# Optimization experiments

Measured on AMD Instinct MI355X. Metric: run time of the kernel, lower is better.

Reference implementation:

```python
import jax, jax.numpy as jnp
import numpy as np

_COOR = [[1,4],[1,5],[1,6],[2,4],[2,6],[3,1],[3,2],[3,3],[3,4],[3,5],[3,6],[3,7],[3,8],[3,9],[4,1],[4,2],[4,3],[4,4],[4,5],[4,6],[4,7],[4,8],[4,9],[5,1],[5,2],[5,3],[5,4],[5,5],[5,6],[5,7],[5,8],[5,9],[6,1],[6,2],[6,3],[6,4],[6,5],[6,6],[6,7],[6,8],[6,9],[7,1],[7,2],[7,3],[7,4],[7,5],[7,6],[7,7],[7,8],[7,9],[8,2],[8,3],[8,4],[8,5],[8,6],[8,7],[8,8],[9,3],[9,4],[9,5],[9,6],[9,7]]
_DIRS = [[1,2,3,4,5,6,7,8,9,10,11,12,13,14,15,16,17,18,19,20,21,22,23,24,25,26,27,28,29,30,31,32,33,34,35,36,37,38,39,40,41,42,43,44,45,46,47,48,49,50,58,52,53,54,55,56,62,60,61,51,57,59],[59,57,51,61,60,62,56,55,54,53,52,58,50,41,32,23,14,49,40,31,22,13,48,39,30,21,12,47,38,29,20,11,46,37,28,19,10,45,36,27,18,9,44,35,26,17,8,43,34,25,16,7,42,33,24,15,6,5,4,3,2,1],[59,57,51,61,60,62,56,55,54,53,52,58,50,49,48,47,46,45,44,43,42,41,40,39,38,37,36,35,34,33,32,31,30,29,28,27,26,25,24,23,22,21,20,19,18,17,16,15,14,13,12,11,10,9,8,7,6,5,4,3,2,1],[1,2,3,4,5,6,15,24,33,42,7,16,25,34,43,8,17,26,35,44,9,18,27,36,45,10,19,28,37,46,11,20,29,38,47,12,21,30,39,48,13,22,31,40,49,14,23,32,41,50,58,52,53,54,55,56,62,60,61,51,57,59]]


def _build_graph():
    D, E = len(_DIRS), len(_COOR)
    Ns = np.zeros((D, E, E), np.float32)
    for di, direction in enumerate(_DIRS):
        for pi in range(E):
            i, j = _COOR[direction[pi] - 1]
            nbrs = {0: [[i, j - 1], [i - 1, j - 1], [i - 1, j]],
                    1: [[i, j + 1], [i - 1, j], [i - 1, j + 1]],
                    2: [[i, j - 1], [i + 1, j - 1], [i + 1, j]],
                    3: [[i, j - 1], [i - 1, j - 1], [i - 1, j]]}[di]
            for nb in nbrs:
                if nb in _COOR:
                    n_idx = _COOR.index(nb) + 1
                    if n_idx in direction[:pi]:
                        Ns[di, pi, direction.index(n_idx)] = 1.0
    perm = np.asarray(_DIRS, np.int32) - 1  # [D,E] electrode index visited at each step
    return jnp.asarray(Ns), jnp.asarray(perm)


def _srnn(x_t, Ns, perm, U_w, U_b, W_w, W_b, sp_bs, P_w, P_b, ps_w, ps_b):
    # x_t: [B,E,C] -> m: [B,HID]
    B, E, _ = x_t.shape
    HID = U_b.shape[1]

    def one_dir(ns, pm, uw, ub, ww, wb, b, pw, pb):
        ux = jnp.einsum('bec,hc->beh', x_t[:, pm], uw) + ub  # [B,E,H] precomputed input term
        H0 = jnp.zeros((B, E, ub.shape[0]), x_t.dtype)

        def step(H, inp):
            ns_row, ux_pi, pi = inp
            # ns_row is nonzero only at already-visited step positions (< pi)
            h_agg = jnp.einsum('e,beh->bh', ns_row, H)
            h = jax.nn.relu(ux_pi + h_agg @ ww.T + wb + b)
            return jax.lax.dynamic_update_slice(H, h[:, None, :], (0, pi, 0)), None

        H, _ = jax.lax.scan(step, H0, (ns, jnp.swapaxes(ux, 0, 1), jnp.arange(E)))
        return jnp.einsum('beh,pe->bhp', H, pw) + pb  # [B,H,P]

    s = jax.vmap(one_dir)(Ns, perm, U_w, U_b, W_w, W_b, sp_bs, P_w, P_b)  # [D,B,H,P]
    s = jnp.moveaxis(s, 0, 2).reshape(B, HID, -1)  # [B,H,D*P]
    return (s @ ps_w.T + ps_b)[..., 0]  # [B,H]


def _trnn(ms, rs_w, rs_b, vs_w, vs_b, bs, pj_w, pj_b):
    # ms: [T,B,H]
    h0 = jnp.zeros(ms.shape[1:], ms.dtype)

    def step(h, m_t):
        h = jax.nn.relu(m_t @ rs_w.T + rs_b + h @ vs_w.T + vs_b + bs)
        return h, h

    _, hs = jax.lax.scan(step, h0, ms)  # [T,B,H]
    return jnp.einsum('tbh,pt->bph', hs, pj_w) + pj_b[None, :, None]  # [B,P,H]


def _forward(x, Ns, perm, U_w, U_b, W_w, W_b, sp_bs, P_w, P_b, ps_w, ps_b,
             f_rs_w, f_rs_b, f_vs_w, f_vs_b, f_bs, f_pj_w, f_pj_b,
             b_rs_w, b_rs_b, b_vs_w, b_vs_b, b_bs, b_pj_w, b_pj_b,
             fp1_w, fp1_b, fp2_w, fp2_b, bp1_w, bp1_b, bp2_w, bp2_b):
    xt = jnp.swapaxes(x, 0, 1)  # [T,B,E,C]
    ms = jax.vmap(lambda xi: _srnn(xi, Ns, perm, U_w, U_b, W_w, W_b, sp_bs,
                                   P_w, P_b, ps_w, ps_b))(xt)  # [T,B,H]
    q_f = _trnn(ms, f_rs_w, f_rs_b, f_vs_w, f_vs_b, f_bs, f_pj_w, f_pj_b)
    q_b = _trnn(ms[::-1], b_rs_w, b_rs_b, b_vs_w, b_vs_b, b_bs, b_pj_w, b_pj_b)
    zf = (q_f @ fp1_w.T + fp1_b)[..., 0]  # [B,Ptp]
    zb = (q_b @ bp1_w.T + bp1_b)[..., 0]
    return zf @ fp2_w.T + fp2_b + zb @ bp2_w.T + bp2_b  # [B,classes]


def setup_inputs() -> dict:
    B, T, E, C = 128, 16, 62, 5
    HID, SPP, TPP, NC, D = 128, 16, 8, 3, 4
    Ns, perm = _build_graph()
    key = jax.random.key(0)
    ks = jax.random.split(key, 34)
    rnd = lambda k, s: (jax.random.normal(k, s, jnp.float32) * 0.05)
    return {
        'x': jax.random.normal(ks[0], (B, T, E, C), jnp.float32),
        'Ns': Ns, 'perm': perm,
        'U_w': rnd(ks[1], (D, HID, C)), 'U_b': rnd(ks[2], (D, HID)),
        'W_w': rnd(ks[3], (D, HID, HID)), 'W_b': rnd(ks[4], (D, HID)),
        'sp_bs': rnd(ks[5], (D, HID)),
        'P_w': rnd(ks[6], (D, SPP, E)), 'P_b': rnd(ks[7], (D, SPP)),
        'ps_w': rnd(ks[8], (1, D * SPP)), 'ps_b': rnd(ks[9], (1,)),
        'f_rs_w': rnd(ks[10], (HID, HID)), 'f_rs_b': rnd(ks[11], (HID,)),
        'f_vs_w': rnd(ks[12], (HID, HID)), 'f_vs_b': rnd(ks[13], (HID,)),
        'f_bs': rnd(ks[14], (HID,)),
        'f_pj_w': rnd(ks[15], (TPP, T)), 'f_pj_b': rnd(ks[16], (TPP,)),
        'b_rs_w': rnd(ks[17], (HID, HID)), 'b_rs_b': rnd(ks[18], (HID,)),
        'b_vs_w': rnd(ks[19], (HID, HID)), 'b_vs_b': rnd(ks[20], (HID,)),
        'b_bs': rnd(ks[21], (HID,)),
        'b_pj_w': rnd(ks[22], (TPP, T)), 'b_pj_b': rnd(ks[23], (TPP,)),
        'fp1_w': rnd(ks[24], (1, HID)), 'fp1_b': rnd(ks[25], (1,)),
        'fp2_w': rnd(ks[26], (NC, TPP)), 'fp2_b': rnd(ks[27], (NC,)),
        'bp1_w': rnd(ks[28], (1, HID)), 'bp1_b': rnd(ks[29], (1,)),
        'bp2_w': rnd(ks[30], (NC, TPP)), 'bp2_b': rnd(ks[31], (NC,)),
    }


def reference(x, Ns, perm, U_w, U_b, W_w, W_b, sp_bs, P_w, P_b, ps_w, ps_b,
              f_rs_w, f_rs_b, f_vs_w, f_vs_b, f_bs, f_pj_w, f_pj_b,
              b_rs_w, b_rs_b, b_vs_w, b_vs_b, b_bs, b_pj_w, b_pj_b,
              fp1_w, fp1_b, fp2_w, fp2_b, bp1_w, bp1_b, bp2_w, bp2_b):
    return _forward(x, Ns, perm, U_w, U_b, W_w, W_b, sp_bs, P_w, P_b, ps_w, ps_b,
                    f_rs_w, f_rs_b, f_vs_w, f_vs_b, f_bs, f_pj_w, f_pj_b,
                    b_rs_w, b_rs_b, b_vs_w, b_vs_b, b_bs, b_pj_w, b_pj_b,
                    fp1_w, fp1_b, fp2_w, fp2_b, bp1_w, bp1_b, bp2_w, bp2_b)
```

## Files before the change

### kernel.cpp

```cpp
#include <hip/hip_runtime.h>

typedef unsigned short u16;
typedef unsigned int   u32;

using bf16x8 = __attribute__((ext_vector_type(8))) short;
using f32x4  = __attribute__((ext_vector_type(4))) float;
using u32x4  = __attribute__((ext_vector_type(4))) unsigned;

__device__ __forceinline__ u32 cvtpk(float lo, float hi) {
  u32 r;
  asm("v_cvt_pk_bf16_f32 %0, %1, %2" : "=v"(r) : "v"(lo), "v"(hi));
  return r;
}
__device__ __forceinline__ bf16x8 pack8(float f0,float f1,float f2,float f3,
                                        float f4,float f5,float f6,float f7) {
  u32x4 t; t[0]=cvtpk(f0,f1); t[1]=cvtpk(f2,f3); t[2]=cvtpk(f4,f5); t[3]=cvtpk(f6,f7);
  return __builtin_bit_cast(bf16x8, t);
}
__device__ __forceinline__ u16 f2bf(float f) {
  u32 u = __float_as_uint(f);
  u32 r = u + 0x7FFFu + ((u >> 16) & 1u);
  return (u16)(r >> 16);
}

struct Sched {
  unsigned v[4][64];
  unsigned char opi[4][64];
  int nslot;
};

constexpr int cCOOR[62][2] = {
  {1,4},{1,5},{1,6},{2,4},{2,6},
  {3,1},{3,2},{3,3},{3,4},{3,5},{3,6},{3,7},{3,8},{3,9},
  {4,1},{4,2},{4,3},{4,4},{4,5},{4,6},{4,7},{4,8},{4,9},
  {5,1},{5,2},{5,3},{5,4},{5,5},{5,6},{5,7},{5,8},{5,9},
  {6,1},{6,2},{6,3},{6,4},{6,5},{6,6},{6,7},{6,8},{6,9},
  {7,1},{7,2},{7,3},{7,4},{7,5},{7,6},{7,7},{7,8},{7,9},
  {8,2},{8,3},{8,4},{8,5},{8,6},{8,7},{8,8},
  {9,3},{9,4},{9,5},{9,6},{9,7}};

constexpr int cDIRS[4][62] = {
  {1,2,3,4,5,6,7,8,9,10,11,12,13,14,15,16,17,18,19,20,21,22,23,24,25,26,27,28,29,30,
   31,32,33,34,35,36,37,38,39,40,41,42,43,44,45,46,47,48,49,50,
   58,52,53,54,55,56,62,60,61,51,57,59},
  {59,57,51,61,60,62,56,55,54,53,52,58,50,41,32,23,14,49,40,31,22,13,48,39,30,21,12,
   47,38,29,20,11,46,37,28,19,10,45,36,27,18,9,44,35,26,17,8,43,34,25,16,7,42,33,24,
   15,6,5,4,3,2,1},
  {59,57,51,61,60,62,56,55,54,53,52,58,50,49,48,47,46,45,44,43,42,41,40,39,38,37,36,
   35,34,33,32,31,30,29,28,27,26,25,24,23,22,21,20,19,18,17,16,15,14,13,12,11,10,9,
   8,7,6,5,4,3,2,1},
  {1,2,3,4,5,6,15,24,33,42,7,16,25,34,43,8,17,26,35,44,9,18,27,36,45,10,19,28,37,46,
   11,20,29,38,47,12,21,30,39,48,13,22,31,40,49,14,23,32,41,50,
   58,52,53,54,55,56,62,60,61,51,57,59}};

constexpr int cOFFS[4][3][2] = {
  {{0,-1},{-1,-1},{-1,0}},
  {{0, 1},{-1, 0},{-1,1}},
  {{0,-1},{ 1,-1},{ 1,0}},
  {{0,-1},{-1,-1},{-1,0}}};

constexpr Sched make_sched() {
  Sched S{};
  int nslot_all = 0;
  for (int d = 0; d < 4; ++d) {
    int pos_of[63] = {};
    for (int p = 0; p < 62; ++p) pos_of[cDIRS[d][p]] = p;
    int nb[62][3] = {}; int nc[62] = {}; int rdcnt[62] = {};
    for (int p = 0; p < 62; ++p) {
      const int e = cDIRS[d][p];
      const int ci = cCOOR[e-1][0], cj = cCOOR[e-1][1];
      for (int o = 0; o < 3; ++o) {
        const int ni = ci + cOFFS[d][o][0], nj = cj + cOFFS[d][o][1];
        int q = 0;
        for (int k2 = 0; k2 < 62; ++k2)
          if (cCOOR[k2][0]==ni && cCOOR[k2][1]==nj) { q = k2+1; break; }
        if (q) { const int qp = pos_of[q];
          if (qp < p) { nb[p][nc[p]] = qp; nc[p] = nc[p]+1; rdcnt[qp] = rdcnt[qp]+1; } }
      }
    }
    int lvl[62] = {};
    for (int p = 0; p < 62; ++p) {
      int m = 0;
      for (int o = 0; o < nc[p]; ++o) if (lvl[nb[p][o]] > m) m = lvl[nb[p][o]];
      lvl[p] = m + 1;
    }
    int ord[62] = {}; int k = 0;
    for (int L = 1; L <= 62; ++L)
      for (int p = 0; p < 62; ++p) if (lvl[p] == L) { ord[k] = p; k = k+1; }
    int slotof[62] = {};
    int rl[20]; int lr[20];
    for (int s = 0; s < 20; ++s) { rl[s] = 0; lr[s] = -1; }
    int nslot = 0, cur_sub = 0;
    int barafter[62] = {};
    int prev_lvl = lvl[ord[0]];
    for (int kk = 0; kk < 62; ++kk) {
      const int p = ord[kk];
      if (lvl[p] != prev_lvl) { barafter[kk-1] = 1; cur_sub = cur_sub+1; prev_lvl = lvl[p]; }
      for (int o = 0; o < nc[p]; ++o) {
        const int s = slotof[nb[p][o]];
        rl[s] = rl[s]-1;
        if (cur_sub > lr[s]) lr[s] = cur_sub;
      }
      int myslot = 31;
      if (rdcnt[p] > 0) {
        int found = -1;
        for (int s = 0; s < nslot; ++s)
          if (rl[s] == 0 && lr[s] < cur_sub) { found = s; break; }
        if (found < 0 && nslot < 19) { found = nslot; nslot = nslot+1; }
        if (found < 0) {
          barafter[kk-1] = 1; cur_sub = cur_sub+1;
          for (int o = 0; o < nc[p]; ++o) {
            const int s = slotof[nb[p][o]];
            if (cur_sub > lr[s]) lr[s] = cur_sub;
          }
          for (int s = 0; s < nslot; ++s)
            if (rl[s] == 0 && lr[s] < cur_sub) { found = s; break; }
        }
        if (found < 0 && nslot < 20) { found = nslot; nslot = nslot+1; }
        if (found < 0) found = 0;
        myslot = found;
        rl[myslot] = rdcnt[p];
        lr[myslot] = -1;
        slotof[p] = myslot;
      }
      S.opi[d][kk] = (unsigned char)p;
      S.v[d][kk] = (unsigned)(cDIRS[d][p]-1)
                 | ((unsigned)myslot << 6)
                 | ((unsigned)nc[p] << 11)
                 | ((unsigned)(nc[p]>0 ? slotof[nb[p][0]] : 0) << 13)
                 | ((unsigned)(nc[p]>1 ? slotof[nb[p][1]] : 0) << 18)
                 | ((unsigned)(nc[p]>2 ? slotof[nb[p][2]] : 0) << 23);
    }
    for (int kk = 0; kk < 62; ++kk) if (barafter[kk]) S.v[d][kk] |= (1u << 28);
    if (nslot > nslot_all) nslot_all = nslot;
  }
  S.nslot = nslot_all;
  return S;
}

constexpr Sched g_sched = make_sched();
static_assert(g_sched.nslot >= 8 && g_sched.nslot <= 20, "slot pressure out of range");
__constant__ Sched c_sched = make_sched();

constexpr int POOL_B     = g_sched.nslot * 4096;
constexpr int WP_OFF     = POOL_B;
constexpr int SRNN_SMEM  = POOL_B + 256;

__global__ __launch_bounds__(256, 2) void srnn_kernel(
    const float* __restrict__ x,    const float* __restrict__ Uw,
    const float* __restrict__ Ub,   const float* __restrict__ Ww,
    const float* __restrict__ Wb,   const float* __restrict__ spbs,
    const float* __restrict__ Pw,   const float* __restrict__ psw,
    float* __restrict__ part)
{
  extern __shared__ __align__(16) char smem[];
  const int tid  = threadIdx.x;
  const int lane = tid & 63, wid = tid >> 6;
  const int l15  = lane & 15, lhi = lane >> 4;
  const int bx = blockIdx.x;
  const int bb = bx & 15, d = (bx >> 4) & 3, tp = bx >> 6;
  const int b0 = bb * 8, t0 = tp * 2;

  float* s_wp = (float*)(smem + WP_OFF);

  if (tid < 62) {
    const int opi = c_sched.opi[d][tid];
    float acc = 0.f;
    for (int q = 0; q < 16; ++q) acc += Pw[(d * 16 + q) * 62 + opi] * psw[d * 16 + q];
    s_wp[tid] = acc;
  }

  bf16x8 wf[2][4];
  float bias[2];
#pragma unroll
  for (int nt = 0; nt < 2; ++nt) {
    const int n = wid * 32 + nt * 16 + l15;
    const float* wr = Ww + (size_t)(d * 128 + n) * 128;
#pragma unroll
    for (int kc = 0; kc < 4; ++kc) {
      float4 lo = *(const float4*)(wr + kc * 32 + lhi * 4);
      float4 hi = *(const float4*)(wr + kc * 32 + lhi * 4 + 16);
      wf[nt][kc] = pack8(lo.x, hi.x, lo.y, hi.y, lo.z, hi.z, lo.w, hi.w);
    }
    bias[nt] = Ub[d * 128 + n] + Wb[d * 128 + n] + spbs[d * 128 + n];
  }

  float u0a=0,u1a=0,u2a=0,u3a=0,u4a=0, u0b=0,u1b=0,u2b=0,u3b=0,u4b=0;
  if (lhi == 0) {
    const float* ua = Uw + (d * 128 + wid * 32 + l15) * 5;
    const float* ub = Uw + (d * 128 + wid * 32 + 16 + l15) * 5;
    u0a=ua[0]; u1a=ua[1]; u2a=ua[2]; u3a=ua[3]; u4a=ua[4];
    u0b=ub[0]; u1b=ub[1]; u2b=ub[2]; u3b=ub[3]; u4b=ub[4];
  }
  const bf16x8 uwf0 = pack8(u0a,u1a,u2a,u3a,u4a,0.f,0.f,0.f);
  const bf16x8 uwf1 = pack8(u0b,u1b,u2b,u3b,u4b,0.f,0.f,0.f);

  __syncthreads();

  const float* xlane = x + (size_t)((b0 + (l15 & 7)) * 16 + (t0 + (l15 >> 3))) * 310;
  const int swz_r = ((l15 & 7) << 4);
  const int wcol  = wid * 64 + l15 * 4;
  const unsigned* scv = c_sched.v[d];

  f32x4 macc0 = {0.f,0.f,0.f,0.f}, macc1 = {0.f,0.f,0.f,0.f};

  auto do_step = [&](unsigned sv, int kidx, float c0, float c1, float c2, float c3, float c4) {
    f32x4 a0 = {bias[0], bias[0], bias[0], bias[0]};
    f32x4 a1 = {bias[1], bias[1], bias[1], bias[1]};
    const int nbc = (int)((sv >> 11) & 3u);
    auto slot_mac = [&](int sl) {
      const char* sb = smem + sl * 4096 + l15 * 256;
#pragma unroll
      for (int kc = 0; kc < 4; ++kc) {
        bf16x8 a = *(const bf16x8*)(sb + ((kc * 64 + lhi * 16) ^ swz_r));
        a0 = __builtin_amdgcn_mfma_f32_16x16x32_bf16(a, wf[0][kc], a0, 0, 0, 0);
        a1 = __builtin_amdgcn_mfma_f32_16x16x32_bf16(a, wf[1][kc], a1, 0, 0, 0);
      }
    };
    if (nbc > 0) slot_mac((int)((sv >> 13) & 31u));
    if (nbc > 1) slot_mac((int)((sv >> 18) & 31u));
    if (nbc > 2) slot_mac((int)((sv >> 23) & 31u));
    bf16x8 xa = pack8(c0, c1, c2, c3, c4, 0.f, 0.f, 0.f);
    a0 = __builtin_amdgcn_mfma_f32_16x16x32_bf16(xa, uwf0, a0, 0, 0, 0);
    a1 = __builtin_amdgcn_mfma_f32_16x16x32_bf16(xa, uwf1, a1, 0, 0, 0);

    const int snew = (int)((sv >> 6) & 31u);
    const float wp = s_wp[kidx];
    float h0r[4], h1r[4];
#pragma unroll
    for (int r = 0; r < 4; ++r) { h0r[r] = fmaxf(a0[r], 0.f); h1r[r] = fmaxf(a1[r], 0.f); }
    if (snew != 31) {
      char* dst = smem + snew * 4096;
#pragma unroll
      for (int r = 0; r < 4; ++r) {
        const int row = lhi * 4 + r;
        *(u32*)(dst + row * 256 + (wcol ^ ((row & 7) << 4))) = cvtpk(h0r[r], h1r[r]);
      }
    }
#pragma unroll
    for (int r = 0; r < 4; ++r) { macc0[r] += h0r[r] * wp; macc1[r] += h1r[r] * wp; }
  };

  for (int pp = 0; pp < 31; ++pp) {
    const unsigned svA = scv[2 * pp];
    const unsigned svB = scv[2 * pp + 1];
    float a0=0,a1=0,a2=0,a3=0,a4=0, b0f=0,b1f=0,b2f=0,b3f=0,b4f=0;
    if (lhi == 0) {
      const float* pA = xlane + (svA & 63u) * 5;
      const float* pB = xlane + (svB & 63u) * 5;
      a0=pA[0]; a1=pA[1]; a2=pA[2]; a3=pA[3]; a4=pA[4];
      b0f=pB[0]; b1f=pB[1]; b2f=pB[2]; b3f=pB[3]; b4f=pB[4];
    }
    do_step(svA, 2 * pp, a0, a1, a2, a3, a4);
    if (svA & (1u << 28)) __syncthreads();
    do_step(svB, 2 * pp + 1, b0f, b1f, b2f, b3f, b4f);
    if (svB & (1u << 28)) __syncthreads();
  }

#pragma unroll
  for (int r = 0; r < 4; ++r) {
    const int row = lhi * 4 + r;
    const int t = t0 + (row >> 3);
    const int brow = b0 + (row & 7);
    const int n0 = wid * 32 + l15;
    float* pp2 = part + (((size_t)d * 16 + t) * 128 + brow) * 128;
    pp2[n0]      = macc0[r];
    pp2[n0 + 16] = macc1[r];
  }
}

constexpr int MS_OFF = 0;
constexpr int HB_OFF = 65536;
constexpr int SW_OFF = HB_OFF + 8704;
constexpr int S2_OFF = SW_OFF + 4096;
constexpr int TRNN_SMEM = S2_OFF + 1024;

__global__ __launch_bounds__(256) void trnn_kernel(
    const float* __restrict__ part, const float* __restrict__ Pb,
    const float* __restrict__ psw,  const float* __restrict__ psb,
    const float* __restrict__ frs, const float* __restrict__ frsb,
    const float* __restrict__ fvs, const float* __restrict__ fvsb,
    const float* __restrict__ fbs, const float* __restrict__ fpj, const float* __restrict__ fpjb,
    const float* __restrict__ brs, const float* __restrict__ brsb,
    const float* __restrict__ bvs, const float* __restrict__ bvsb,
    const float* __restrict__ bbs, const float* __restrict__ bpj, const float* __restrict__ bpjb,
    const float* __restrict__ fp1w, const float* __restrict__ fp1b,
    const float* __restrict__ fp2w, const float* __restrict__ fp2b,
    const float* __restrict__ bp1w, const float* __restrict__ bp1b,
    const float* __restrict__ bp2w, const float* __restrict__ bp2b,
    float* __restrict__ out)
{
  extern __shared__ __align__(16) char smem[];
  const int tid = threadIdx.x;
  const int lane = tid & 63, wid = tid >> 6;
  const int l15 = lane & 15, lhi = lane >> 4;
  const int dir = blockIdx.x & 1;
  const int b0 = (blockIdx.x >> 1) * 16;

  const float* rs  = dir ? brs  : frs;
  const float* rsb = dir ? brsb : frsb;
  const float* vs  = dir ? bvs  : fvs;
  const float* vsb = dir ? bvsb : fvsb;
  const float* bs  = dir ? bbs  : fbs;
  const float* w1  = dir ? bp1w : fp1w;

  {
    const int tq = tid >> 4, bq = tid & 15;
    float c0 = psb[0];
#pragma unroll
    for (int i = 0; i < 16; ++i) {
      float4 pb4 = *(const float4*)(Pb + i * 4);
      float4 pw4 = *(const float4*)(psw + i * 4);
      c0 += pb4.x*pw4.x + pb4.y*pw4.y + pb4.z*pw4.z + pb4.w*pw4.w;
    }
    const size_t base = ((size_t)tq * 128 + b0 + bq) * 128;
    const float* p0 = part + base;
    const float* p1 = part + base + 262144;
    const float* p2 = part + base + 2 * 262144;
    const float* p3 = part + base + 3 * 262144;
    char* mrow = smem + MS_OFF + (tq * 16 + bq) * 256;
    const int sz = (bq & 7) << 4;
    for (int h4 = 0; h4 < 32; ++h4) {
      float4 v0 = *(const float4*)(p0 + h4 * 4);
      float4 v1 = *(const float4*)(p1 + h4 * 4);
      float4 v2 = *(const float4*)(p2 + h4 * 4);
      float4 v3 = *(const float4*)(p3 + h4 * 4);
      float s0 = v0.x + v1.x + v2.x + v3.x + c0;
      float s1 = v0.y + v1.y + v2.y + v3.y + c0;
      float s2 = v0.z + v1.z + v2.z + v3.z + c0;
      float s3 = v0.w + v1.w + v2.w + v3.w + c0;
      *(u32*)(mrow + ((h4 * 8) ^ sz))     = cvtpk(s0, s1);
      *(u32*)(mrow + ((h4 * 8 + 4) ^ sz)) = cvtpk(s2, s3);
    }
  }

  bf16x8 rf[2][4], vf[2][4];
  float bias[2], w1a, w1b;
#pragma unroll
  for (int nt = 0; nt < 2; ++nt) {
    const int n = wid * 32 + nt * 16 + l15;
#pragma unroll
    for (int kc = 0; kc < 4; ++kc) {
      float4 ra = *(const float4*)(rs + (size_t)n * 128 + kc * 32 + lhi * 8);
      float4 rb = *(const float4*)(rs + (size_t)n * 128 + kc * 32 + lhi * 8 + 4);
      rf[nt][kc] = pack8(ra.x, ra.y, ra.z, ra.w, rb.x, rb.y, rb.z, rb.w);
      float4 lo = *(const float4*)(vs + (size_t)n * 128 + kc * 32 + lhi * 4);
      float4 hi = *(const float4*)(vs + (size_t)n * 128 + kc * 32 + lhi * 4 + 16);
      vf[nt][kc] = pack8(lo.x, hi.x, lo.y, hi.y, lo.z, hi.z, lo.w, hi.w);
    }
    bias[nt] = rsb[n] + vsb[n] + bs[n];
  }
  w1a = w1[wid * 32 + l15];
  w1b = w1[wid * 32 + 16 + l15];

  for (int i = tid; i < 2176; i += 256) *(u16*)(smem + HB_OFF + i * 2) = 0;
  __syncthreads();

  float* sredw = (float*)(smem + SW_OFF);
  float* sred2 = (float*)(smem + S2_OFF);

  int cur = 0;
  for (int tt2 = 0; tt2 < 16; ++tt2) {
    const int tt = dir ? (15 - tt2) : tt2;
    f32x4 am0 = {bias[0],bias[0],bias[0],bias[0]};
    f32x4 am1 = {bias[1],bias[1],bias[1],bias[1]};
    f32x4 ah0 = {0.f,0.f,0.f,0.f}, ah1 = {0.f,0.f,0.f,0.f};
    const char* msrow = smem + MS_OFF + (tt * 16 + l15) * 256;
    const int msz = (l15 & 7) << 4;
#pragma unroll
    for (int kc = 0; kc < 4; ++kc) {
      bf16x8 ma = *(const bf16x8*)(msrow + ((kc * 64 + lhi * 16) ^ msz));
      bf16x8 ha = *(const bf16x8*)(smem + HB_OFF + (cur * 16 + l15) * 272 + kc * 64 + lhi * 16);
      am0 = __builtin_amdgcn_mfma_f32_16x16x32_bf16(ma, rf[0][kc], am0, 0, 0, 0);
      ah0 = __builtin_amdgcn_mfma_f32_16x16x32_bf16(ha, vf[0][kc], ah0, 0, 0, 0);
      am1 = __builtin_amdgcn_mfma_f32_16x16x32_bf16(ma, rf[1][kc], am1, 0, 0, 0);
      ah1 = __builtin_amdgcn_mfma_f32_16x16x32_bf16(ha, vf[1][kc], ah1, 0, 0, 0);
    }
    float pr[4];
#pragma unroll
    for (int r = 0; r < 4; ++r) {
      const int row = lhi * 4 + r;
      float h0 = fmaxf(am0[r] + ah0[r], 0.f);
      float h1 = fmaxf(am1[r] + ah1[r], 0.f);
      *(u32*)(smem + HB_OFF + ((cur ^ 1) * 16 + row) * 272 + wid * 64 + l15 * 4) = cvtpk(h0, h1);
      pr[r] = h0 * w1a + h1 * w1b;
    }
#pragma unroll
    for (int r = 0; r < 4; ++r) {
      float p = pr[r];
      p += __shfl_xor(p, 1);
      p += __shfl_xor(p, 2);
      p += __shfl_xor(p, 4);
      p += __shfl_xor(p, 8);
      if (l15 == 0) sredw[(tt2 * 16 + lhi * 4 + r) * 4 + wid] = p;
    }
    __syncthreads();
    cur ^= 1;
  }

  {
    const int tq = tid >> 4, bq = tid & 15;
    const float* sw = sredw + (tq * 16 + bq) * 4;
    sred2[tq * 16 + bq] = sw[0] + sw[1] + sw[2] + sw[3];
  }
  __syncthreads();

  if (tid < 48) {
    const int b = tid / 3, c = tid % 3;
    const float* p1w = dir ? bp1w : fp1w;
    const float* p1b = dir ? bp1b : fp1b;
    const float* p2w = dir ? bp2w : fp2w;
    const float* p2b = dir ? bp2b : fp2b;
    const float* pj  = dir ? bpj  : fpj;
    const float* pjb = dir ? bpjb : fpjb;
    float S1 = 0.f;
    for (int h = 0; h < 128; ++h) S1 += p1w[h];
    float val = p2b[c];
    for (int p = 0; p < 8; ++p) val += (pjb[p] * S1 + p1b[0]) * p2w[c * 8 + p];
    for (int t2 = 0; t2 < 16; ++t2) {
      float g = 0.f;
      for (int p = 0; p < 8; ++p) g += p2w[c * 8 + p] * pj[p * 16 + t2];
      val += sred2[t2 * 16 + b] * g;
    }
    atomicAdd(out + (b0 + b) * 3 + c, val);
  }
}

extern "C" void kernel_launch(void* const* d_in, const int* in_sizes, int n_in,
                              void* d_out, int out_size, void* d_ws, size_t ws_size,
                              hipStream_t stream)
{
  (void)in_sizes; (void)n_in; (void)ws_size;
  const float* x    = (const float*)d_in[0];
  const float* Uw   = (const float*)d_in[3];
  const float* Ub   = (const float*)d_in[4];
  const float* Ww   = (const float*)d_in[5];
  const float* Wb   = (const float*)d_in[6];
  const float* spbs = (const float*)d_in[7];
  const float* Pw   = (const float*)d_in[8];
  const float* Pb   = (const float*)d_in[9];
  const float* psw  = (const float*)d_in[10];
  const float* psb  = (const float*)d_in[11];
  const float* frs  = (const float*)d_in[12];
  const float* frsb = (const float*)d_in[13];
  const float* fvs  = (const float*)d_in[14];
  const float* fvsb = (const float*)d_in[15];
  const float* fbs  = (const float*)d_in[16];
  const float* fpj  = (const float*)d_in[17];
  const float* fpjb = (const float*)d_in[18];
  const float* brs  = (const float*)d_in[19];
  const float* brsb = (const float*)d_in[20];
  const float* bvs  = (const float*)d_in[21];
  const float* bvsb = (const float*)d_in[22];
  const float* bbs  = (const float*)d_in[23];
  const float* bpj  = (const float*)d_in[24];
  const float* bpjb = (const float*)d_in[25];
  const float* fp1w = (const float*)d_in[26];
  const float* fp1b = (const float*)d_in[27];
  const float* fp2w = (const float*)d_in[28];
  const float* fp2b = (const float*)d_in[29];
  const float* bp1w = (const float*)d_in[30];
  const float* bp1b = (const float*)d_in[31];
  const float* bp2w = (const float*)d_in[32];
  const float* bp2b = (const float*)d_in[33];

  float* part = (float*)d_ws;

  hipFuncSetAttribute((const void*)srnn_kernel,
                      hipFuncAttributeMaxDynamicSharedMemorySize, SRNN_SMEM);
  hipFuncSetAttribute((const void*)trnn_kernel,
                      hipFuncAttributeMaxDynamicSharedMemorySize, TRNN_SMEM);

  hipMemsetAsync(d_out, 0, (size_t)out_size * sizeof(float), stream);

  srnn_kernel<<<dim3(512), dim3(256), SRNN_SMEM, stream>>>(
      x, Uw, Ub, Ww, Wb, spbs, Pw, psw, part);
  trnn_kernel<<<dim3(16), dim3(256), TRNN_SMEM, stream>>>(part, Pb, psw, psb,
      frs, frsb, fvs, fvsb, fbs, fpj, fpjb,
      brs, brsb, bvs, bvsb, bbs, bpj, bpjb,
      fp1w, fp1b, fp2w, fp2b, bp1w, bp1b, bp2w, bp2b,
      (float*)d_out);
}
```

Before: 89.67 us.

## Fully unroll SRNN schedule at compile time and split partial reduction into kernel

```diff
diff --git a/kernel.cpp b/kernel.cpp
--- a/kernel.cpp
+++ b/kernel.cpp
@@ -1,4 +1,5 @@
 #include <hip/hip_runtime.h>
+#include <utility>
 
 typedef unsigned short u16;
 typedef unsigned int   u32;
@@ -142,120 +143,177 @@
 static_assert(g_sched.nslot >= 8 && g_sched.nslot <= 20, "slot pressure out of range");
 __constant__ Sched c_sched = make_sched();
 
-constexpr int POOL_B     = g_sched.nslot * 4096;
-constexpr int WP_OFF     = POOL_B;
-constexpr int SRNN_SMEM  = POOL_B + 256;
-
-__global__ __launch_bounds__(256, 2) void srnn_kernel(
-    const float* __restrict__ x,    const float* __restrict__ Uw,
-    const float* __restrict__ Ub,   const float* __restrict__ Ww,
-    const float* __restrict__ Wb,   const float* __restrict__ spbs,
-    const float* __restrict__ Pw,   const float* __restrict__ psw,
-    float* __restrict__ part)
+constexpr int POOL_B    = g_sched.nslot * 4096;
+constexpr int SRNN_SMEM = POOL_B + 256;
+
+template <int D, int K>
+__device__ __forceinline__ void do_step(
+    char* smem, const float* s_wp,
+    const bf16x8 (&wf)[2][4], const bf16x8& uwf0, const bf16x8& uwf1,
+    float bias0, float bias1,
+    const u32 (&xr)[16][3], const int (&bad)[4],
+    const u32 (&rdv)[4], const u32 (&wav)[4],
+    f32x4& macc0, f32x4& macc1)
+{
+  constexpr unsigned sv = g_sched.v[D][K];
+  constexpr int snew = (int)((sv >> 6) & 31u);
+  constexpr int nbc  = (int)((sv >> 11) & 3u);
+  constexpr int sl0  = (int)((sv >> 13) & 31u);
+  constexpr int sl1  = (int)((sv >> 18) & 31u);
+  constexpr int sl2  = (int)((sv >> 23) & 31u);
+  constexpr int g    = K & 3;
+  constexpr int js   = K >> 2;
+
+  u32 r0 = (u32)__builtin_amdgcn_ds_bpermute(bad[g], (int)xr[js][0]);
+  u32 r1 = (u32)__builtin_amdgcn_ds_bpermute(bad[g], (int)xr[js][1]);
+  u32 r2 = (u32)__builtin_amdgcn_ds_bpermute(bad[g], (int)xr[js][2]);
+
+  f32x4 a0 = {bias0, bias0, bias0, bias0};
+  f32x4 a1 = {bias1, bias1, bias1, bias1};
+
+  if constexpr (nbc > 0) {
+#pragma unroll
+    for (int kc = 0; kc < 4; ++kc) {
+      bf16x8 a = *(const bf16x8*)(smem + sl0 * 4096 + rdv[kc]);
+      a0 = __builtin_amdgcn_mfma_f32_16x16x32_bf16(a, wf[0][kc], a0, 0, 0, 0);
+      a1 = __builtin_amdgcn_mfma_f32_16x16x32_bf16(a, wf[1][kc], a1, 0, 0, 0);
+    }
+  }
+  if constexpr (nbc > 1) {
+#pragma unroll
+    for (int kc = 0; kc < 4; ++kc) {
+      bf16x8 a = *(const bf16x8*)(smem + sl1 * 4096 + rdv[kc]);
+      a0 = __builtin_amdgcn_mfma_f32_16x16x32_bf16(a, wf[0][kc], a0, 0, 0, 0);
+      a1 = __builtin_amdgcn_mfma_f32_16x16x32_bf16(a, wf[1][kc], a1, 0, 0, 0);
+    }
+  }
+  if constexpr (nbc > 2) {
+#pragma unroll
+    for (int kc = 0; kc < 4; ++kc) {
+      bf16x8 a = *(const bf16x8*)(smem + sl2 * 4096 + rdv[kc]);
+      a0 = __builtin_amdgcn_mfma_f32_16x16x32_bf16(a, wf[0][kc], a0, 0, 0, 0);
+      a1 = __builtin_amdgcn_mfma_f32_16x16x32_bf16(a, wf[1][kc], a1, 0, 0, 0);
+    }
+  }
+  {
+    u32x4 xv; xv[0] = r0; xv[1] = r1; xv[2] = r2; xv[3] = 0;
+    bf16x8 xa = __builtin_bit_cast(bf16x8, xv);
+    a0 = __builtin_amdgcn_mfma_f32_16x16x32_bf16(xa, uwf0, a0, 0, 0, 0);
+    a1 = __builtin_amdgcn_mfma_f32_16x16x32_bf16(xa, uwf1, a1, 0, 0, 0);
+  }
+
+  const float wp = s_wp[K];
+  float h0[4], h1[4];
+#pragma unroll
+  for (int r = 0; r < 4; ++r) { h0[r] = fmaxf(a0[r], 0.f); h1[r] = fmaxf(a1[r], 0.f); }
+  if constexpr (snew != 31) {
+#pragma unroll
+    for (int r = 0; r < 4; ++r)
+      *(u32*)(smem + snew * 4096 + wav[r]) = cvtpk(h0[r], h1[r]);
+  }
+#pragma unroll
+  for (int r = 0; r < 4; ++r) { macc0[r] += h0[r] * wp; macc1[r] += h1[r] * wp; }
+
+  if constexpr ((sv >> 28) & 1u) __syncthreads();
+}
+
+template <int D, int... Ks>
+__device__ __forceinline__ void run_steps(
+    std::integer_sequence<int, Ks...>,
+    char* smem, const float* s_wp,
+    const bf16x8 (&wf)[2][4], const bf16x8& uwf0, const bf16x8& uwf1,
+    float bias0, float bias1,
+    const u32 (&xr)[16][3], const int (&bad)[4],
+    const u32 (&rdv)[4], const u32 (&wav)[4],
+    f32x4& macc0, f32x4& macc1)
+{
+  (do_step<D, Ks>(smem, s_wp, wf, uwf0, uwf1, bias0, bias1,
+                  xr, bad, rdv, wav, macc0, macc1), ...);
+}
+
+template <int D>
+__device__ __noinline__ void srnn_body(
+    const float* __restrict__ x,  const float* __restrict__ Uw,
+    const float* __restrict__ Ub, const float* __restrict__ Ww,
+    const float* __restrict__ Wb, const float* __restrict__ spbs,
+    const float* __restrict__ Pw, const float* __restrict__ psw,
+    float* __restrict__ part, int bx)
 {
   extern __shared__ __align__(16) char smem[];
   const int tid  = threadIdx.x;
   const int lane = tid & 63, wid = tid >> 6;
   const int l15  = lane & 15, lhi = lane >> 4;
-  const int bx = blockIdx.x;
-  const int bb = bx & 15, d = (bx >> 4) & 3, tp = bx >> 6;
+  const int bb = bx & 15, tp = bx >> 6;
   const int b0 = bb * 8, t0 = tp * 2;
 
-  float* s_wp = (float*)(smem + WP_OFF);
+  float* s_wp = (float*)(smem + POOL_B);
 
   if (tid < 62) {
-    const int opi = c_sched.opi[d][tid];
+    const int opi = c_sched.opi[D][tid];
     float acc = 0.f;
-    for (int q = 0; q < 16; ++q) acc += Pw[(d * 16 + q) * 62 + opi] * psw[d * 16 + q];
+    for (int q = 0; q < 16; ++q) acc += Pw[(D * 16 + q) * 62 + opi] * psw[D * 16 + q];
     s_wp[tid] = acc;
   }
 
   bf16x8 wf[2][4];
-  float bias[2];
+  float bias0, bias1;
 #pragma unroll
   for (int nt = 0; nt < 2; ++nt) {
     const int n = wid * 32 + nt * 16 + l15;
-    const float* wr = Ww + (size_t)(d * 128 + n) * 128;
+    const float* wr = Ww + (size_t)(D * 128 + n) * 128;
 #pragma unroll
     for (int kc = 0; kc < 4; ++kc) {
       float4 lo = *(const float4*)(wr + kc * 32 + lhi * 4);
       float4 hi = *(const float4*)(wr + kc * 32 + lhi * 4 + 16);
       wf[nt][kc] = pack8(lo.x, hi.x, lo.y, hi.y, lo.z, hi.z, lo.w, hi.w);
     }
-    bias[nt] = Ub[d * 128 + n] + Wb[d * 128 + n] + spbs[d * 128 + n];
+    float bnt = Ub[D * 128 + n] + Wb[D * 128 + n] + spbs[D * 128 + n];
+    if (nt == 0) bias0 = bnt; else bias1 = bnt;
   }
 
   float u0a=0,u1a=0,u2a=0,u3a=0,u4a=0, u0b=0,u1b=0,u2b=0,u3b=0,u4b=0;
   if (lhi == 0) {
-    const float* ua = Uw + (d * 128 + wid * 32 + l15) * 5;
-    const float* ub = Uw + (d * 128 + wid * 32 + 16 + l15) * 5;
+    const float* ua = Uw + (D * 128 + wid * 32 + l15) * 5;
+    const float* ub = Uw + (D * 128 + wid * 32 + 16 + l15) * 5;
     u0a=ua[0]; u1a=ua[1]; u2a=ua[2]; u3a=ua[3]; u4a=ua[4];
     u0b=ub[0]; u1b=ub[1]; u2b=ub[2]; u3b=ub[3]; u4b=ub[4];
   }
   const bf16x8 uwf0 = pack8(u0a,u1a,u2a,u3a,u4a,0.f,0.f,0.f);
   const bf16x8 uwf1 = pack8(u0b,u1b,u2b,u3b,u4b,0.f,0.f,0.f);
 
+  const float* xlane = x + (size_t)((b0 + (l15 & 7)) * 16 + (t0 + (l15 >> 3))) * 310;
+  u32 xr[16][3];
+#pragma unroll
+  for (int j = 0; j < 16; ++j) {
+    const int e = (int)(c_sched.v[D][j * 4 + lhi] & 63u);
+    const float* xp = xlane + e * 5;
+    float x0 = xp[0], x1 = xp[1], x2 = xp[2], x3 = xp[3], x4 = xp[4];
+    xr[j][0] = cvtpk(x0, x1);
+    xr[j][1] = cvtpk(x2, x3);
+    xr[j][2] = cvtpk(x4, 0.f);
+  }
+
+  const int swz_r = ((l15 & 7) << 4);
+  u32 rdv[4], wav[4];
+#pragma unroll
+  for (int kc = 0; kc < 4; ++kc)
+    rdv[kc] = (u32)(l15 * 256 + ((kc * 64 + lhi * 16) ^ swz_r));
+  const int wcol = wid * 64 + l15 * 4;
+#pragma unroll
+  for (int r = 0; r < 4; ++r) {
+    const int row = lhi * 4 + r;
+    wav[r] = (u32)(row * 256 + (wcol ^ ((row & 7) << 4)));
+  }
+  int bad[4];
+#pragma unroll
+  for (int i = 0; i < 4; ++i) bad[i] = (i * 16 + l15) * 4;
+
   __syncthreads();
 
-  const float* xlane = x + (size_t)((b0 + (l15 & 7)) * 16 + (t0 + (l15 >> 3))) * 310;
-  const int swz_r = ((l15 & 7) << 4);
-  const int wcol  = wid * 64 + l15 * 4;
-  const unsigned* scv = c_sched.v[d];
-
   f32x4 macc0 = {0.f,0.f,0.f,0.f}, macc1 = {0.f,0.f,0.f,0.f};
-
-  auto do_step = [&](unsigned sv, int kidx, float c0, float c1, float c2, float c3, float c4) {
-    f32x4 a0 = {bias[0], bias[0], bias[0], bias[0]};
-    f32x4 a1 = {bias[1], bias[1], bias[1], bias[1]};
-    const int nbc = (int)((sv >> 11) & 3u);
-    auto slot_mac = [&](int sl) {
-      const char* sb = smem + sl * 4096 + l15 * 256;
-#pragma unroll
-      for (int kc = 0; kc < 4; ++kc) {
-        bf16x8 a = *(const bf16x8*)(sb + ((kc * 64 + lhi * 16) ^ swz_r));
-        a0 = __builtin_amdgcn_mfma_f32_16x16x32_bf16(a, wf[0][kc], a0, 0, 0, 0);
-        a1 = __builtin_amdgcn_mfma_f32_16x16x32_bf16(a, wf[1][kc], a1, 0, 0, 0);
-      }
-    };
-    if (nbc > 0) slot_mac((int)((sv >> 13) & 31u));
-    if (nbc > 1) slot_mac((int)((sv >> 18) & 31u));
-    if (nbc > 2) slot_mac((int)((sv >> 23) & 31u));
-    bf16x8 xa = pack8(c0, c1, c2, c3, c4, 0.f, 0.f, 0.f);
-    a0 = __builtin_amdgcn_mfma_f32_16x16x32_bf16(xa, uwf0, a0, 0, 0, 0);
-    a1 = __builtin_amdgcn_mfma_f32_16x16x32_bf16(xa, uwf1, a1, 0, 0, 0);
-
-    const int snew = (int)((sv >> 6) & 31u);
-    const float wp = s_wp[kidx];
-    float h0r[4], h1r[4];
-#pragma unroll
-    for (int r = 0; r < 4; ++r) { h0r[r] = fmaxf(a0[r], 0.f); h1r[r] = fmaxf(a1[r], 0.f); }
-    if (snew != 31) {
-      char* dst = smem + snew * 4096;
-#pragma unroll
-      for (int r = 0; r < 4; ++r) {
-        const int row = lhi * 4 + r;
-        *(u32*)(dst + row * 256 + (wcol ^ ((row & 7) << 4))) = cvtpk(h0r[r], h1r[r]);
-      }
-    }
-#pragma unroll
-    for (int r = 0; r < 4; ++r) { macc0[r] += h0r[r] * wp; macc1[r] += h1r[r] * wp; }
-  };
-
-  for (int pp = 0; pp < 31; ++pp) {
-    const unsigned svA = scv[2 * pp];
-    const unsigned svB = scv[2 * pp + 1];
-    float a0=0,a1=0,a2=0,a3=0,a4=0, b0f=0,b1f=0,b2f=0,b3f=0,b4f=0;
-    if (lhi == 0) {
-      const float* pA = xlane + (svA & 63u) * 5;
-      const float* pB = xlane + (svB & 63u) * 5;
-      a0=pA[0]; a1=pA[1]; a2=pA[2]; a3=pA[3]; a4=pA[4];
-      b0f=pB[0]; b1f=pB[1]; b2f=pB[2]; b3f=pB[3]; b4f=pB[4];
-    }
-    do_step(svA, 2 * pp, a0, a1, a2, a3, a4);
-    if (svA & (1u << 28)) __syncthreads();
-    do_step(svB, 2 * pp + 1, b0f, b1f, b2f, b3f, b4f);
-    if (svB & (1u << 28)) __syncthreads();
-  }
+  run_steps<D>(std::make_integer_sequence<int, 62>{},
+               smem, s_wp, wf, uwf0, uwf1, bias0, bias1,
+               xr, bad, rdv, wav, macc0, macc1);
 
 #pragma unroll
   for (int r = 0; r < 4; ++r) {
@@ -263,10 +321,43 @@
     const int t = t0 + (row >> 3);
     const int brow = b0 + (row & 7);
     const int n0 = wid * 32 + l15;
-    float* pp2 = part + (((size_t)d * 16 + t) * 128 + brow) * 128;
-    pp2[n0]      = macc0[r];
-    pp2[n0 + 16] = macc1[r];
-  }
+    float* pp = part + (((size_t)D * 16 + t) * 128 + brow) * 128;
+    pp[n0]      = macc0[r];
+    pp[n0 + 16] = macc1[r];
+  }
+}
+
+__global__ __launch_bounds__(256, 2) void srnn_kernel(
+    const float* __restrict__ x,  const float* __restrict__ Uw,
+    const float* __restrict__ Ub, const float* __restrict__ Ww,
+    const float* __restrict__ Wb, const float* __restrict__ spbs,
+    const float* __restrict__ Pw, const float* __restrict__ psw,
+    float* __restrict__ part)
+{
+  const int bx = blockIdx.x;
+  switch ((bx >> 4) & 3) {
+    case 0: srnn_body<0>(x, Uw, Ub, Ww, Wb, spbs, Pw, psw, part, bx); break;
+    case 1: srnn_body<1>(x, Uw, Ub, Ww, Wb, spbs, Pw, psw, part, bx); break;
+    case 2: srnn_body<2>(x, Uw, Ub, Ww, Wb, spbs, Pw, psw, part, bx); break;
+    default: srnn_body<3>(x, Uw, Ub, Ww, Wb, spbs, Pw, psw, part, bx); break;
+  }
+}
+
+__global__ __launch_bounds__(256) void reduce_ms_kernel(
+    const float* __restrict__ part, const float* __restrict__ Pb,
+    const float* __restrict__ psw,  const float* __restrict__ psb,
+    u16* __restrict__ msbf, float* __restrict__ out)
+{
+  const int tid = threadIdx.x;
+  if (blockIdx.x == 0 && tid < 128) {
+    float3 z = {0.f, 0.f, 0.f};
+    *(float3*)(out + tid * 3) = z;
+  }
+  const int idx = blockIdx.x * 256 + tid;
+  float c0 = psb[0];
+  for (int i = 0; i < 64; ++i) c0 += Pb[i] * psw[i];
+  float s = c0 + part[idx] + part[262144 + idx] + part[2 * 262144 + idx] + part[3 * 262144 + idx];
+  msbf[idx] = f2bf(s);
 }
 
 constexpr int MS_OFF = 0;
@@ -276,8 +367,7 @@
 constexpr int TRNN_SMEM = S2_OFF + 1024;
 
 __global__ __launch_bounds__(256) void trnn_kernel(
-    const float* __restrict__ part, const float* __restrict__ Pb,
-    const float* __restrict__ psw,  const float* __restrict__ psb,
+    const u16* __restrict__ msbf,
     const float* __restrict__ frs, const float* __restrict__ frsb,
     const float* __restrict__ fvs, const float* __restrict__ fvsb,
     const float* __restrict__ fbs, const float* __restrict__ fpj, const float* __restrict__ fpjb,
@@ -306,31 +396,16 @@
 
   {
     const int tq = tid >> 4, bq = tid & 15;
-    float c0 = psb[0];
-#pragma unroll
-    for (int i = 0; i < 16; ++i) {
-      float4 pb4 = *(const float4*)(Pb + i * 4);
-      float4 pw4 = *(const float4*)(psw + i * 4);
-      c0 += pb4.x*pw4.x + pb4.y*pw4.y + pb4.z*pw4.z + pb4.w*pw4.w;
-    }
-    const size_t base = ((size_t)tq * 128 + b0 + bq) * 128;
-    const float* p0 = part + base;
-    const float* p1 = part + base + 262144;
-    const float* p2 = part + base + 2 * 262144;
-    const float* p3 = part + base + 3 * 262144;
+    const u16* mg = msbf + ((size_t)tq * 128 + b0 + bq) * 128;
     char* mrow = smem + MS_OFF + (tq * 16 + bq) * 256;
     const int sz = (bq & 7) << 4;
-    for (int h4 = 0; h4 < 32; ++h4) {
-      float4 v0 = *(const float4*)(p0 + h4 * 4);
-      float4 v1 = *(const float4*)(p1 + h4 * 4);
-      float4 v2 = *(const float4*)(p2 + h4 * 4);
-      float4 v3 = *(const float4*)(p3 + h4 * 4);
-      float s0 = v0.x + v1.x + v2.x + v3.x + c0;
-      float s1 = v0.y + v1.y + v2.y + v3.y + c0;
-      float s2 = v0.z + v1.z + v2.z + v3.z + c0;
-      float s3 = v0.w + v1.w + v2.w + v3.w + c0;
-      *(u32*)(mrow + ((h4 * 8) ^ sz))     = cvtpk(s0, s1);
-      *(u32*)(mrow + ((h4 * 8 + 4) ^ sz)) = cvtpk(s2, s3);
+#pragma unroll
+    for (int q = 0; q < 16; ++q) {
+      uint4 v = *(const uint4*)(mg + q * 8);
+      *(u32*)(mrow + ((q * 16)      ^ sz)) = v.x;
+      *(u32*)(mrow + ((q * 16 + 4)  ^ sz)) = v.y;
+      *(u32*)(mrow + ((q * 16 + 8)  ^ sz)) = v.z;
+      *(u32*)(mrow + ((q * 16 + 12) ^ sz)) = v.w;
     }
   }
 
@@ -430,7 +505,7 @@
                               void* d_out, int out_size, void* d_ws, size_t ws_size,
                               hipStream_t stream)
 {
-  (void)in_sizes; (void)n_in; (void)ws_size;
+  (void)in_sizes; (void)n_in; (void)out_size; (void)ws_size;
   const float* x    = (const float*)d_in[0];
   const float* Uw   = (const float*)d_in[3];
   const float* Ub   = (const float*)d_in[4];
@@ -464,18 +539,20 @@
   const float* bp2w = (const float*)d_in[32];
   const float* bp2b = (const float*)d_in[33];
 
-  float* part = (float*)d_ws;
+  char* ws = (char*)d_ws;
+  float* part = (float*)ws;
+  u16*   msbf = (u16*)(ws + 4194304);
 
   hipFuncSetAttribute((const void*)srnn_kernel,
                       hipFuncAttributeMaxDynamicSharedMemorySize, SRNN_SMEM);
   hipFuncSetAttribute((const void*)trnn_kernel,
                       hipFuncAttributeMaxDynamicSharedMemorySize, TRNN_SMEM);
 
-  hipMemsetAsync(d_out, 0, (size_t)out_size * sizeof(float), stream);
-
   srnn_kernel<<<dim3(512), dim3(256), SRNN_SMEM, stream>>>(
       x, Uw, Ub, Ww, Wb, spbs, Pw, psw, part);
-  trnn_kernel<<<dim3(16), dim3(256), TRNN_SMEM, stream>>>(part, Pb, psw, psb,
+  reduce_ms_kernel<<<dim3(1024), dim3(256), 0, stream>>>(
+      part, Pb, psw, psb, msbf, (float*)d_out);
+  trnn_kernel<<<dim3(16), dim3(256), TRNN_SMEM, stream>>>(msbf,
       frs, frsb, fvs, fvsb, fbs, fpj, fpjb,
       brs, brsb, bvs, bvsb, bbs, bpj, bpjb,
       fp1w, fp1b, fp2w, fp2b, bp1w, bp1b, bp2w, bp2b,
```

New measurement: 76.31 us. 1.18x faster.
